# Performance work log

Measured on AMD Instinct MI355X. Metric: run time of the kernel, lower is better.

## Reference

```python
import jax, jax.numpy as jnp
import numpy as np

B, S, E, NH = 2, 2048, 1024, 4
DH = E // NH
EPS = 1e-6  # backend stabilization eps and layernorm eps


def setup_inputs() -> dict:
    key = jax.random.key(0)
    ks = jax.random.split(key, 7)
    q = jax.random.normal(ks[0], (B, S, E), jnp.float32)
    k = jax.random.normal(ks[1], (B, S, E), jnp.float32)
    v = jax.random.normal(ks[2], (B, S, E), jnp.float32)
    # Gate Dense layers: kernel zero-init in the module; use small random so the
    # math is non-trivial. Biases follow the module's inits.
    igate_kernel = 0.02 * jax.random.normal(ks[3], (3 * E, NH), jnp.float32)
    fgate_kernel = 0.02 * jax.random.normal(ks[4], (3 * E, NH), jnp.float32)
    igate_bias = 0.1 * jax.random.normal(ks[5], (NH,), jnp.float32)
    fgate_bias = jnp.linspace(3.0, 6.0, NH, dtype=jnp.float32)  # bias_linspace_init(3,6)
    outnorm_weight = jnp.ones((NH, DH), jnp.float32)
    return {
        "q": q, "k": k, "v": v,
        "igate_kernel": igate_kernel, "igate_bias": igate_bias,
        "fgate_kernel": fgate_kernel, "fgate_bias": fgate_bias,
        "outnorm_weight": outnorm_weight,
    }


def _mlstm_parallel_stabilized(q, k, v, ig, fg):
    # q,k,v: (B,NH,S,DH); ig,fg: (B,NH,S) gate pre-activations
    log_fg = jax.nn.log_sigmoid(fg)                     # (B,NH,S)
    c = jnp.cumsum(log_fg, axis=-1)                     # cumulative forget gates
    # log decay matrix: entry (i,j) = sum_{s=j+1..i} log_fg[s] = c[i]-c[j], causal
    log_fg_mat = c[..., :, None] - c[..., None, :]      # (B,NH,S,S)
    causal = jnp.tril(jnp.ones((S, S), bool))
    log_D = jnp.where(causal, log_fg_mat + ig[..., None, :], -jnp.inf)
    max_log_D = jnp.max(log_D, axis=-1, keepdims=True)  # (B,NH,S,1)
    D = jnp.exp(log_D - max_log_D)                      # stabilized decay matrix
    qk = jnp.einsum("bhsd,bhtd->bhst", q, k) / jnp.sqrt(jnp.float32(DH))
    C = qk * D                                          # (B,NH,S,S)
    normalizer = jnp.maximum(jnp.abs(jnp.sum(C, axis=-1, keepdims=True)),
                             jnp.exp(-max_log_D))
    C_norm = C / (normalizer + EPS)
    return jnp.einsum("bhst,bhtd->bhsd", C_norm, v)     # (B,NH,S,DH)


def reference(q, k, v, igate_kernel, igate_bias, fgate_kernel, fgate_bias, outnorm_weight):
    gate_in = jnp.concatenate([q, k, v], axis=-1)       # (B,S,3E)
    ig = gate_in @ igate_kernel + igate_bias            # (B,S,NH)
    fg = gate_in @ fgate_kernel + fgate_bias            # (B,S,NH)
    qh = q.reshape(B, S, NH, DH).transpose(0, 2, 1, 3)  # (B,NH,S,DH)
    kh = k.reshape(B, S, NH, DH).transpose(0, 2, 1, 3)
    vh = v.reshape(B, S, NH, DH).transpose(0, 2, 1, 3)
    h = _mlstm_parallel_stabilized(qh, kh, vh,
                                   ig.transpose(0, 2, 1), fg.transpose(0, 2, 1))
    h = h.transpose(0, 2, 1, 3)                          # (B,S,NH,DH)
    # MultiHeadLayerNorm: normalize over DH per head, weight only (no bias)
    mean = jnp.mean(h, axis=-1, keepdims=True)
    var = jnp.var(h, axis=-1, keepdims=True)
    h_norm = (h - mean) * jax.lax.rsqrt(var + EPS) * outnorm_weight
    return h_norm.reshape(B, S, E)
```

## Files before the change

### kernel.cpp

```cpp
#include <hip/hip_runtime.h>
#include <hip/hip_bf16.h>
#include <math.h>

#define B_  2
#define S_  2048
#define E_  1024
#define NH_ 4
#define DH_ 256
#define EPSF 1e-6f

typedef __attribute__((ext_vector_type(4)))  short  s16x4;
typedef __attribute__((ext_vector_type(8)))  short  s16x8;
typedef __attribute__((ext_vector_type(8)))  __bf16 bf16x8;
typedef __attribute__((ext_vector_type(4)))  float  f32x4;
typedef __attribute__((ext_vector_type(16))) float  f32x16;

static __device__ __forceinline__ short f2bf(float f) {
    unsigned u = __builtin_bit_cast(unsigned, f);
    u = (u + 0x7FFFu + ((u >> 16) & 1u)) >> 16;
    return (short)u;
}

static __device__ __forceinline__ void gload16(const void* g, void* l) {
    __builtin_amdgcn_global_load_lds(
        (__attribute__((address_space(1))) void*)g,
        (__attribute__((address_space(3))) void*)l, 16, 0, 0);
}

static __device__ __host__ __forceinline__ int chunk_prefix(int N) {
    int k = N >> 3, r = N & 7;
    return 4 * k * (k + 1) + r * (k + 1);
}

__global__ __launch_bounds__(256)
void prep_kernel(const float* __restrict__ q, const float* __restrict__ k,
                 const float* __restrict__ v,
                 const float* __restrict__ igk, const float* __restrict__ igb,
                 const float* __restrict__ fgk, const float* __restrict__ fgb,
                 short* __restrict__ qbf, short* __restrict__ kbf,
                 short* __restrict__ vt,
                 float* __restrict__ ig_ws, float* __restrict__ fg_ws) {
    const int bid = blockIdx.x;
    if (bid < 512) {
        int wid = threadIdx.x >> 6, lane = threadIdx.x & 63;
        int row0 = (bid * 4 + wid) * 2;
        int b = row0 >> 11;
        int s0 = row0 & 2047;
        float accI[2][4] = {};
        float accF[2][4] = {};
        const float* srcs[3] = {q, k, v};
        short* dsts[2] = {qbf, kbf};
#pragma unroll
        for (int p = 0; p < 3; p++) {
            const float* src = srcs[p] + ((long)b * S_ + s0) * E_;
#pragma unroll
            for (int c = 0; c < 4; c++) {
                int e = c * 256 + lane * 4;
                float4 x0 = *(const float4*)(src + e);
                float4 x1 = *(const float4*)(src + E_ + e);
                if (p < 2) {
                    s16x4 o0, o1;
                    o0[0] = f2bf(x0.x); o0[1] = f2bf(x0.y); o0[2] = f2bf(x0.z); o0[3] = f2bf(x0.w);
                    o1[0] = f2bf(x1.x); o1[1] = f2bf(x1.y); o1[2] = f2bf(x1.z); o1[3] = f2bf(x1.w);
                    long db = ((long)(b * NH_ + c) * S_ + s0) * DH_ + lane * 4;
                    *(s16x4*)(dsts[p] + db) = o0;
                    *(s16x4*)(dsts[p] + db + DH_) = o1;
                }
                const float4* wi = (const float4*)(igk + (long)(p * E_ + e) * 4);
                const float4* wf = (const float4*)(fgk + (long)(p * E_ + e) * 4);
                float xs0[4] = {x0.x, x0.y, x0.z, x0.w};
                float xs1[4] = {x1.x, x1.y, x1.z, x1.w};
#pragma unroll
                for (int j = 0; j < 4; j++) {
                    float4 wij = wi[j], wfj = wf[j];
                    accI[0][0] += xs0[j] * wij.x; accI[0][1] += xs0[j] * wij.y;
                    accI[0][2] += xs0[j] * wij.z; accI[0][3] += xs0[j] * wij.w;
                    accF[0][0] += xs0[j] * wfj.x; accF[0][1] += xs0[j] * wfj.y;
                    accF[0][2] += xs0[j] * wfj.z; accF[0][3] += xs0[j] * wfj.w;
                    accI[1][0] += xs1[j] * wij.x; accI[1][1] += xs1[j] * wij.y;
                    accI[1][2] += xs1[j] * wij.z; accI[1][3] += xs1[j] * wij.w;
                    accF[1][0] += xs1[j] * wfj.x; accF[1][1] += xs1[j] * wfj.y;
                    accF[1][2] += xs1[j] * wfj.z; accF[1][3] += xs1[j] * wfj.w;
                }
            }
        }
#pragma unroll
        for (int r = 0; r < 2; r++) {
#pragma unroll
            for (int hh = 0; hh < 4; hh++) {
                float aI = accI[r][hh], aF = accF[r][hh];
                for (int m = 1; m < 64; m <<= 1) { aI += __shfl_xor(aI, m); aF += __shfl_xor(aF, m); }
                if (lane == 0) {
                    ig_ws[((long)(b * NH_ + hh)) * S_ + s0 + r] = aI + igb[hh];
                    fg_ws[((long)(b * NH_ + hh)) * S_ + s0 + r] = aF + fgb[hh];
                }
            }
        }
    } else {
        __shared__ short tile[64][66];
        int b2 = bid - 512;
        int dt = b2 & 3, st = (b2 >> 2) & 31, hh = (b2 >> 7) & 3, b = b2 >> 9;
        int t = threadIdx.x;
#pragma unroll
        for (int rep = 0; rep < 16; rep++) {
            int idx = t + rep * 256;
            int ts = idx >> 6, td = idx & 63;
            float x = v[((long)b * S_ + st * 64 + ts) * E_ + hh * DH_ + dt * 64 + td];
            tile[ts][td] = f2bf(x);
        }
        __syncthreads();
        long obase = ((long)(b * NH_ + hh) * DH_ + dt * 64) * S_ + st * 64;
#pragma unroll
        for (int rep = 0; rep < 8; rep++) {
            int idx = t + rep * 256;
            int dd = idx >> 5, sp = (idx & 31) * 2;
            short2 val;
            val.x = tile[sp][dd];
            val.y = tile[sp + 1][dd];
            *(short2*)(vt + obase + (long)dd * S_ + sp) = val;
        }
    }
}

__global__ __launch_bounds__(256)
void scan_kernel(const float* __restrict__ ig_ws, const float* __restrict__ fg_ws,
                 float* __restrict__ c_ws, float* __restrict__ a_ws,
                 float* __restrict__ M_ws) {
    __shared__ float wsum[4], wmax[4];
    int seq = blockIdx.x;
    int tid = threadIdx.x, w = tid >> 6, lane = tid & 63;
    long base = (long)seq * S_;
    float carryC = 0.f, carryM = -INFINITY;
    for (int ch = 0; ch < S_ / 256; ch++) {
        int s = ch * 256 + tid;
        float fgv = fg_ws[base + s];
        float lf = (fgv > 0.f) ? -log1pf(expf(-fgv)) : (fgv - log1pf(expf(fgv)));
        float x = lf;
        for (int d = 1; d < 64; d <<= 1) { float t = __shfl_up(x, d); if (lane >= d) x += t; }
        if (lane == 63) wsum[w] = x;
        __syncthreads();
        float pre = carryC;
        for (int j = 0; j < w; j++) pre += wsum[j];
        float c = pre + x;
        float a = ig_ws[base + s] - c;
        float m = a;
        for (int d = 1; d < 64; d <<= 1) { float t = __shfl_up(m, d); if (lane >= d) m = fmaxf(m, t); }
        if (lane == 63) wmax[w] = m;
        __syncthreads();
        float prem = carryM;
        for (int j = 0; j < w; j++) prem = fmaxf(prem, wmax[j]);
        float M = fmaxf(prem, m);
        c_ws[base + s] = c;
        a_ws[base + s] = a;
        M_ws[base + s] = M;
        carryC += wsum[0] + wsum[1] + wsum[2] + wsum[3];
        carryM = fmaxf(fmaxf(fmaxf(carryM, wmax[0]), fmaxf(wmax[1], wmax[2])), wmax[3]);
        __syncthreads();
    }
}

__global__ __launch_bounds__(256)
void mlstm_pipe(const short* __restrict__ qbf, const short* __restrict__ kbf,
                const short* __restrict__ vt,
                const float* __restrict__ a_ws, const float* __restrict__ M_ws,
                float* __restrict__ num_ws, float* __restrict__ den_ws) {
    __shared__ __align__(16) char LDSb[139264];

    const int bid = blockIdx.x;
    const int seq = bid & 7;
    const int local = 79 - (bid >> 3);
    int qt = 0;
#pragma unroll
    for (int t = 1; t < 32; t++) if (chunk_prefix(t) <= local) qt = t;
    const int chunk = local - chunk_prefix(qt);
    const int kt0 = chunk * 8;
    const int kt1 = min(kt0 + 8, qt + 1);

    const int tid = threadIdx.x;
    const int w  = tid >> 6;
    const int rg = w & 1;
    const int ct = w >> 1;
    const int l  = tid & 63;
    const int l31 = l & 31;
    const int h5  = l >> 5;

    const long seqbase = (long)seq * S_ * DH_;
    const long gbase = (long)seq * S_;
    const int i0 = qt * 64;

    const char* kseq = (const char*)(kbf + seqbase);
    const char* vseq = (const char*)(vt + seqbase);

    int preK[8], preV[8];
#pragma unroll
    for (int i = 0; i < 8; i++) {
        int r = w * 16 + i * 2 + (l >> 5);
        preK[i] = r * 512 + (((l & 31) * 16) ^ ((r & 7) << 4));
        int d = w * 64 + i * 8 + (l >> 3);
        preV[i] = d * (S_ * 2) + (((l & 7) * 16) ^ ((d & 7) << 4));
    }

    float Mi[16];
#pragma unroll
    for (int reg = 0; reg < 16; reg++) {
        int rowL = 32 * rg + (reg & 3) + 8 * (reg >> 2) + 4 * h5;
        Mi[reg] = M_ws[gbase + i0 + rowL];
    }

    {
        short* Qlds = (short*)LDSb;
#pragma unroll
        for (int rep = 0; rep < 8; rep++) {
            int idx = tid + rep * 256;
            int r = idx >> 5, c = idx & 31;
            s16x8 val = *(const s16x8*)(qbf + seqbase + (long)(i0 + r) * DH_ + c * 8);
            int byte = (r * 512 + c * 16) ^ ((r & 7) << 4);
            *(s16x8*)((char*)Qlds + byte) = val;
        }
    }
    __syncthreads();
    bf16x8 qfrag[16];
    {
        int qrow = 32 * rg + l31;
        int qswz = (qrow & 7) << 4;
#pragma unroll
        for (int dc = 0; dc < 16; dc++)
            qfrag[dc] = *(const bf16x8*)((const char*)LDSb + ((qrow * 512 + dc * 32 + h5 * 16) ^ qswz));
    }
    __syncthreads();

    {
        const char* ks = kseq + (long)kt0 * 64 * 512;
        const char* vs = vseq + (long)kt0 * 128;
        char* kd = LDSb + w * 8192;
        char* vd = LDSb + 65536 + w * 8192;
#pragma unroll
        for (int i = 0; i < 8; i++) gload16(ks + preK[i], kd + i * 1024);
#pragma unroll
        for (int i = 0; i < 8; i++) gload16(vs + preV[i], vd + i * 1024);
    }
    __syncthreads();

    f32x16 oacc[4] = {};
    float denacc[16] = {};

    for (int kt = kt0; kt < kt1; kt++) {
        const int cur = (kt - kt0) & 1;
        const int j0 = kt * 64;

        if (kt + 1 < kt1) {
            const char* ks = kseq + (long)(kt + 1) * 64 * 512;
            const char* vs = vseq + (long)(kt + 1) * 128;
            char* kd = LDSb + (cur ^ 1) * 32768 + w * 8192;
            char* vd = LDSb + 65536 + (cur ^ 1) * 32768 + w * 8192;
#pragma unroll
            for (int i = 0; i < 8; i++) gload16(ks + preK[i], kd + i * 1024);
#pragma unroll
            for (int i = 0; i < 8; i++) gload16(vs + preV[i], vd + i * 1024);
        }

        const char* Klds  = LDSb + cur * 32768;
        const char* Vtlds = LDSb + 65536 + cur * 32768;
        char* Plds = LDSb + 131072;

        float aj = a_ws[gbase + j0 + 32 * ct + l31];

        f32x16 sacc = {};
        {
            int j = 32 * ct + l31;
            int jswz = (j & 7) << 4;
            int jbase = j * 512;
#pragma unroll
            for (int dc = 0; dc < 16; dc++) {
                bf16x8 kf = *(const bf16x8*)(Klds + ((jbase + dc * 32 + h5 * 16) ^ jswz));
                sacc = __builtin_amdgcn_mfma_f32_32x32x16_bf16(qfrag[dc], kf, sacc, 0, 0, 0);
            }
        }

        {
            int jg = j0 + 32 * ct + l31;
#pragma unroll
            for (int reg = 0; reg < 16; reg++) {
                int rowL = 32 * rg + (reg & 3) + 8 * (reg >> 2) + 4 * h5;
                float p = sacc[reg] * 0.0625f * __expf(aj - Mi[reg]);
                if (jg > i0 + rowL) p = 0.f;
                denacc[reg] += p;
                int byte = (rowL * 128 + (32 * ct + l31) * 2) ^ ((rowL & 7) << 4);
                *(short*)(Plds + byte) = f2bf(p);
            }
        }
        __syncthreads();

        bf16x8 pfrag[4];
        {
            int prow = 32 * rg + l31;
            int pswz = (prow & 7) << 4;
#pragma unroll
            for (int k4 = 0; k4 < 4; k4++)
                pfrag[k4] = *(const bf16x8*)(Plds + ((prow * 128 + k4 * 32 + h5 * 16) ^ pswz));
        }
#pragma unroll
        for (int dt = 0; dt < 4; dt++) {
            int d = 128 * ct + 32 * dt + l31;
            int dbase = d * 128, dswz = (d & 7) << 4;
#pragma unroll
            for (int k4 = 0; k4 < 4; k4++) {
                bf16x8 vf = *(const bf16x8*)(Vtlds + ((dbase + k4 * 32 + h5 * 16) ^ dswz));
                oacc[dt] = __builtin_amdgcn_mfma_f32_32x32x16_bf16(pfrag[k4], vf, oacc[dt], 0, 0, 0);
            }
        }
        __syncthreads();
    }

    const long nbase = (long)bid * 64 * 256;
#pragma unroll
    for (int reg = 0; reg < 16; reg++) {
        float dsum = denacc[reg];
        dsum += __shfl_xor(dsum, 1);
        dsum += __shfl_xor(dsum, 2);
        dsum += __shfl_xor(dsum, 4);
        dsum += __shfl_xor(dsum, 8);
        dsum += __shfl_xor(dsum, 16);
        int rowL = 32 * rg + (reg & 3) + 8 * (reg >> 2) + 4 * h5;
        if (l31 == 0) den_ws[(long)bid * 128 + ct * 64 + rowL] = dsum;
    }
#pragma unroll
    for (int dt = 0; dt < 4; dt++) {
#pragma unroll
        for (int reg = 0; reg < 16; reg++) {
            int rowL = 32 * rg + (reg & 3) + 8 * (reg >> 2) + 4 * h5;
            num_ws[nbase + (long)rowL * 256 + 128 * ct + 32 * dt + l31] = oacc[dt][reg];
        }
    }
}

__global__ __launch_bounds__(256)
void reduce_kernel(const float* __restrict__ num_ws, const float* __restrict__ den_ws,
                   const float* __restrict__ c_ws, const float* __restrict__ M_ws,
                   const float* __restrict__ onw, float* __restrict__ out) {
    const int bid = blockIdx.x;
    const int seq = bid & 7;
    const int qh = bid >> 3;
    const int qt = qh >> 1;
    const int half = qh & 1;
    const int h = seq & 3;
    const int b = seq >> 2;
    const int nc = (qt >> 3) + 1;
    const int lbase = chunk_prefix(qt);
    const int w = threadIdx.x >> 6;
    const int l = threadIdx.x & 63;
    const long gbase = (long)seq * S_;

    float4 w4 = *(const float4*)(onw + h * DH_ + l * 4);

    for (int rr = 0; rr < 8; rr++) {
        int row = half * 32 + w * 8 + rr;
        int s = qt * 64 + row;
        float4 acc = {0.f, 0.f, 0.f, 0.f};
        float dsum = 0.f;
        for (int c = 0; c < nc; c++) {
            const long cid = (long)((79 - (lbase + c)) << 3) + seq;
            const float4 p = *(const float4*)(num_ws + cid * 16384 + (long)row * 256 + l * 4);
            acc.x += p.x; acc.y += p.y; acc.z += p.z; acc.w += p.w;
            dsum += den_ws[cid * 128 + row] + den_ws[cid * 128 + 64 + row];
        }
        float lb = __expf(-c_ws[gbase + s] - M_ws[gbase + s]);
        float inv = 1.f / (fmaxf(fabsf(dsum), lb) + EPSF);
        float4 x = {acc.x * inv, acc.y * inv, acc.z * inv, acc.w * inv};
        float sum = x.x + x.y + x.z + x.w;
        sum += __shfl_xor(sum, 1); sum += __shfl_xor(sum, 2); sum += __shfl_xor(sum, 4);
        sum += __shfl_xor(sum, 8); sum += __shfl_xor(sum, 16); sum += __shfl_xor(sum, 32);
        float mean = sum * (1.f / 256.f);
        float vx = x.x - mean, vy = x.y - mean, vz = x.z - mean, vw = x.w - mean;
        float vs = vx * vx + vy * vy + vz * vz + vw * vw;
        vs += __shfl_xor(vs, 1); vs += __shfl_xor(vs, 2); vs += __shfl_xor(vs, 4);
        vs += __shfl_xor(vs, 8); vs += __shfl_xor(vs, 16); vs += __shfl_xor(vs, 32);
        float rstd = rsqrtf(vs * (1.f / 256.f) + EPSF);
        float4 o;
        o.x = vx * rstd * w4.x; o.y = vy * rstd * w4.y;
        o.z = vz * rstd * w4.z; o.w = vw * rstd * w4.w;
        *(float4*)(out + ((long)b * S_ + s) * E_ + h * DH_ + l * 4) = o;
    }
}

__global__ __launch_bounds__(256)
void mlstm_mono(const short* __restrict__ qbf, const short* __restrict__ kbf,
                const short* __restrict__ vt,
                const float* __restrict__ a_ws, const float* __restrict__ M_ws,
                const float* __restrict__ c_ws, const float* __restrict__ onw,
                float* __restrict__ out) {
    __shared__ __align__(16) short Klds[64 * 256];
    __shared__ __align__(16) short Vtlds[256 * 64];
    short* Plds = Klds;

    const int bid = blockIdx.x;
    const int seq = bid & 7;
    const int qt = bid >> 3;
    const int h = seq & 3;
    const int b = seq >> 2;
    const int tid = threadIdx.x;
    const int w = tid >> 6;
    const int l = tid & 63;
    const int l15 = l & 15;
    const int g = l >> 4;

    const long seqbase = (long)seq * S_ * DH_;
    const long gbase = (long)seq * S_;
    const int i0 = qt * 64;

    float Mi_r[4], ci_r[4];
#pragma unroll
    for (int r = 0; r < 4; r++) {
        int il = 16 * w + 4 * g + r;
        Mi_r[r] = M_ws[gbase + i0 + il];
        ci_r[r] = c_ws[gbase + i0 + il];
    }
#pragma unroll
    for (int rep = 0; rep < 8; rep++) {
        int idx = tid + rep * 256;
        int r = idx >> 5, c = idx & 31;
        s16x8 val = *(const s16x8*)(qbf + seqbase + (long)(i0 + r) * DH_ + c * 8);
        int byte = (r * 512 + c * 16) ^ ((r & 7) << 4);
        *(s16x8*)((char*)Klds + byte) = val;
    }
    __syncthreads();
    bf16x8 qfrag[8];
#pragma unroll
    for (int dc = 0; dc < 8; dc++) {
        int r = 16 * w + l15;
        int byte = (r * 512 + (8 * g + 32 * dc) * 2) ^ ((r & 7) << 4);
        qfrag[dc] = *(const bf16x8*)((const char*)Klds + byte);
    }
    __syncthreads();

    const f32x4 fzero = {0.f, 0.f, 0.f, 0.f};
    f32x4 oacc[16];
#pragma unroll
    for (int dt = 0; dt < 16; dt++) oacc[dt] = fzero;
    float den[4] = {0.f, 0.f, 0.f, 0.f};

    const int nkt = qt + 1;
    for (int kt = 0; kt < nkt; kt++) {
        const int j0 = kt * 64;
#pragma unroll
        for (int rep = 0; rep < 8; rep++) {
            int idx = tid + rep * 256;
            int r = idx >> 5, c = idx & 31;
            s16x8 val = *(const s16x8*)(kbf + seqbase + (long)(j0 + r) * DH_ + c * 8);
            int byte = (r * 512 + c * 16) ^ ((r & 7) << 4);
            *(s16x8*)((char*)Klds + byte) = val;
        }
#pragma unroll
        for (int rep = 0; rep < 8; rep++) {
            int idx = tid + rep * 256;
            int d = idx >> 3, c = idx & 7;
            s16x8 val = *(const s16x8*)(vt + seqbase + (long)d * S_ + j0 + c * 8);
            int byte = (d * 128 + c * 16) ^ ((d & 7) << 4);
            *(s16x8*)((char*)Vtlds + byte) = val;
        }
        float aj_ct[4];
#pragma unroll
        for (int ct = 0; ct < 4; ct++) aj_ct[ct] = a_ws[gbase + j0 + 16 * ct + l15];
        __syncthreads();

        f32x4 sacc[4];
#pragma unroll
        for (int ct = 0; ct < 4; ct++) sacc[ct] = fzero;
#pragma unroll
        for (int dc = 0; dc < 8; dc++) {
#pragma unroll
            for (int ct = 0; ct < 4; ct++) {
                int j = 16 * ct + l15;
                int byte = (j * 512 + (8 * g + 32 * dc) * 2) ^ ((j & 7) << 4);
                bf16x8 kf = *(const bf16x8*)((const char*)Klds + byte);
                sacc[ct] = __builtin_amdgcn_mfma_f32_16x16x32_bf16(qfrag[dc], kf, sacc[ct], 0, 0, 0);
            }
        }
        __syncthreads();

        const bool diag = (kt == qt);
#pragma unroll
        for (int ct = 0; ct < 4; ct++) {
            int jl = 16 * ct + l15;
            float aj = aj_ct[ct];
#pragma unroll
            for (int r = 0; r < 4; r++) {
                int il = 16 * w + 4 * g + r;
                float p = sacc[ct][r] * 0.0625f * __expf(aj - Mi_r[r]);
                if (diag && jl > il) p = 0.f;
                den[r] += p;
                int byte = (il * 128 + jl * 2) ^ ((il & 7) << 4);
                *(short*)((char*)Plds + byte) = f2bf(p);
            }
        }
        __syncthreads();

        bf16x8 pfrag[2];
#pragma unroll
        for (int jc = 0; jc < 2; jc++) {
            int i = 16 * w + l15;
            int byte = (i * 128 + (8 * g + 32 * jc) * 2) ^ ((i & 7) << 4);
            pfrag[jc] = *(const bf16x8*)((const char*)Plds + byte);
        }
#pragma unroll
        for (int dt = 0; dt < 16; dt++) {
#pragma unroll
            for (int jc = 0; jc < 2; jc++) {
                int d = 16 * dt + l15;
                int byte = (d * 128 + (8 * g + 32 * jc) * 2) ^ ((d & 7) << 4);
                bf16x8 vf = *(const bf16x8*)((const char*)Vtlds + byte);
                oacc[dt] = __builtin_amdgcn_mfma_f32_16x16x32_bf16(pfrag[jc], vf, oacc[dt], 0, 0, 0);
            }
        }
        __syncthreads();
    }

#pragma unroll
    for (int r = 0; r < 4; r++) {
        float dsum = den[r];
        dsum += __shfl_xor(dsum, 1);
        dsum += __shfl_xor(dsum, 2);
        dsum += __shfl_xor(dsum, 4);
        dsum += __shfl_xor(dsum, 8);
        int il = 16 * w + 4 * g + r;
        float lb = __expf(-ci_r[r] - Mi_r[r]);
        float inv = 1.f / (fmaxf(fabsf(dsum), lb) + EPSF);
        float x[16];
        float sum = 0.f;
#pragma unroll
        for (int dt = 0; dt < 16; dt++) { x[dt] = oacc[dt][r] * inv; sum += x[dt]; }
        sum += __shfl_xor(sum, 1); sum += __shfl_xor(sum, 2);
        sum += __shfl_xor(sum, 4); sum += __shfl_xor(sum, 8);
        float mean = sum * (1.f / 256.f);
        float vs = 0.f;
#pragma unroll
        for (int dt = 0; dt < 16; dt++) { float dx = x[dt] - mean; vs += dx * dx; }
        vs += __shfl_xor(vs, 1); vs += __shfl_xor(vs, 2);
        vs += __shfl_xor(vs, 4); vs += __shfl_xor(vs, 8);
        float rstd = rsqrtf(vs * (1.f / 256.f) + EPSF);
        long orow = ((long)b * S_ + i0 + il) * E_ + h * DH_;
#pragma unroll
        for (int dt = 0; dt < 16; dt++) {
            int d = 16 * dt + l15;
            out[orow + d] = (x[dt] - mean) * rstd * onw[h * DH_ + d];
        }
    }
}

extern "C" void kernel_launch(void* const* d_in, const int* in_sizes, int n_in,
                              void* d_out, int out_size, void* d_ws, size_t ws_size,
                              hipStream_t stream) {
    const float* q   = (const float*)d_in[0];
    const float* k   = (const float*)d_in[1];
    const float* v   = (const float*)d_in[2];
    const float* igk = (const float*)d_in[3];
    const float* igb = (const float*)d_in[4];
    const float* fgk = (const float*)d_in[5];
    const float* fgb = (const float*)d_in[6];
    const float* onw = (const float*)d_in[7];
    float* out = (float*)d_out;

    char* ws = (char*)d_ws;
    float* ig_ws = (float*)(ws);
    float* fg_ws = (float*)(ws + (64  << 10));
    float* c_ws  = (float*)(ws + (128 << 10));
    float* a_ws  = (float*)(ws + (192 << 10));
    float* M_ws  = (float*)(ws + (256 << 10));
    short* qbf   = (short*)(ws + (1L  << 20));
    short* kbf   = (short*)(ws + (9L  << 20));
    short* vtb   = (short*)(ws + (17L << 20));
    float* num_ws = (float*)(ws + (25L << 20));
    float* den_ws = (float*)(ws + (65L << 20));

    prep_kernel<<<1536, 256, 0, stream>>>(q, k, v, igk, igb, fgk, fgb,
                                          qbf, kbf, vtb, ig_ws, fg_ws);
    scan_kernel<<<8, 256, 0, stream>>>(ig_ws, fg_ws, c_ws, a_ws, M_ws);

    if (ws_size >= (66L << 20)) {
        mlstm_pipe  <<<640, 256, 0, stream>>>(qbf, kbf, vtb, a_ws, M_ws, num_ws, den_ws);
        reduce_kernel<<<512, 256, 0, stream>>>(num_ws, den_ws, c_ws, M_ws, onw, out);
    } else {
        mlstm_mono  <<<256, 256, 0, stream>>>(qbf, kbf, vtb, a_ws, M_ws, c_ws, onw, out);
    }
}
```

Baseline: 151.1 us.

## Replace double-buffered K/V staging with single buffer to cut LDS footprint

Drops the double-buffered K/V tiles in shared memory for a single buffer, shrinking LDS from about 136KB to 72KB per block. This could let two blocks share a CU, raising occupancy. The cost is that the prefetch of the next K/V tile no longer overlaps with compute, so each iteration loads and then waits at a barrier before its MFMAs. The hidden loop tail presumably synchronizes before the buffer is overwritten.

```diff
diff --git a/kernel.cpp b/kernel.cpp
--- a/kernel.cpp
+++ b/kernel.cpp
@@ -160,11 +160,11 @@
 }
 
 __global__ __launch_bounds__(256)
-void mlstm_pipe(const short* __restrict__ qbf, const short* __restrict__ kbf,
-                const short* __restrict__ vt,
-                const float* __restrict__ a_ws, const float* __restrict__ M_ws,
-                float* __restrict__ num_ws, float* __restrict__ den_ws) {
-    __shared__ __align__(16) char LDSb[139264];
+void mlstm_sb1(const short* __restrict__ qbf, const short* __restrict__ kbf,
+               const short* __restrict__ vt,
+               const float* __restrict__ a_ws, const float* __restrict__ M_ws,
+               float* __restrict__ num_ws, float* __restrict__ den_ws) {
+    __shared__ __align__(16) char LDSb[73728];
 
     const int bid = blockIdx.x;
     const int seq = bid & 7;
@@ -207,16 +207,13 @@
         Mi[reg] = M_ws[gbase + i0 + rowL];
     }
 
-    {
-        short* Qlds = (short*)LDSb;
-#pragma unroll
-        for (int rep = 0; rep < 8; rep++) {
-            int idx = tid + rep * 256;
-            int r = idx >> 5, c = idx & 31;
-            s16x8 val = *(const s16x8*)(qbf + seqbase + (long)(i0 + r) * DH_ + c * 8);
-            int byte = (r * 512 + c * 16) ^ ((r & 7) << 4);
-            *(s16x8*)((char*)Qlds + byte) = val;
-        }
+#pragma unroll
+    for (int rep = 0; rep < 8; rep++) {
+        int idx = tid + rep * 256;
+        int r = idx >> 5, c = idx & 31;
+        s16x8 val = *(const s16x8*)(qbf + seqbase + (long)(i0 + r) * DH_ + c * 8);
+        int byte = (r * 512 + c * 16) ^ ((r & 7) << 4);
+        *(s16x8*)(LDSb + byte) = val;
     }
     __syncthreads();
     bf16x8 qfrag[16];
@@ -225,45 +222,32 @@
         int qswz = (qrow & 7) << 4;
 #pragma unroll
         for (int dc = 0; dc < 16; dc++)
-            qfrag[dc] = *(const bf16x8*)((const char*)LDSb + ((qrow * 512 + dc * 32 + h5 * 16) ^ qswz));
-    }
-    __syncthreads();
-
-    {
-        const char* ks = kseq + (long)kt0 * 64 * 512;
-        const char* vs = vseq + (long)kt0 * 128;
-        char* kd = LDSb + w * 8192;
-        char* vd = LDSb + 65536 + w * 8192;
-#pragma unroll
-        for (int i = 0; i < 8; i++) gload16(ks + preK[i], kd + i * 1024);
-#pragma unroll
-        for (int i = 0; i < 8; i++) gload16(vs + preV[i], vd + i * 1024);
+            qfrag[dc] = *(const bf16x8*)(LDSb + ((qrow * 512 + dc * 32 + h5 * 16) ^ qswz));
     }
     __syncthreads();
 
     f32x16 oacc[4] = {};
     float denacc[16] = {};
 
+    const char* Klds  = LDSb;
+    const char* Vtlds = LDSb + 32768;
+    char* Plds = LDSb + 65536;
+
     for (int kt = kt0; kt < kt1; kt++) {
-        const int cur = (kt - kt0) & 1;
         const int j0 = kt * 64;
 
-        if (kt + 1 < kt1) {
-            const char* ks = kseq + (long)(kt + 1) * 64 * 512;
-            const char* vs = vseq + (long)(kt + 1) * 128;
-            char* kd = LDSb + (cur ^ 1) * 32768 + w * 8192;
-            char* vd = LDSb + 65536 + (cur ^ 1) * 32768 + w * 8192;
+        {
+            const char* ks = kseq + (long)j0 * 512;
+            const char* vs = vseq + (long)j0 * 2;
+            char* kd = LDSb + w * 8192;
+            char* vd = LDSb + 32768 + w * 8192;
 #pragma unroll
             for (int i = 0; i < 8; i++) gload16(ks + preK[i], kd + i * 1024);
 #pragma unroll
             for (int i = 0; i < 8; i++) gload16(vs + preV[i], vd + i * 1024);
         }
-
-        const char* Klds  = LDSb + cur * 32768;
-        const char* Vtlds = LDSb + 65536 + cur * 32768;
-        char* Plds = LDSb + 131072;
-
         float aj = a_ws[gbase + j0 + 32 * ct + l31];
+        __syncthreads();
 
         f32x16 sacc = {};
         {
@@ -577,7 +561,7 @@
     scan_kernel<<<8, 256, 0, stream>>>(ig_ws, fg_ws, c_ws, a_ws, M_ws);
 
     if (ws_size >= (66L << 20)) {
-        mlstm_pipe  <<<640, 256, 0, stream>>>(qbf, kbf, vtb, a_ws, M_ws, num_ws, den_ws);
+        mlstm_sb1   <<<640, 256, 0, stream>>>(qbf, kbf, vtb, a_ws, M_ws, num_ws, den_ws);
         reduce_kernel<<<512, 256, 0, stream>>>(num_ws, den_ws, c_ws, M_ws, onw, out);
     } else {
         mlstm_mono  <<<256, 256, 0, stream>>>(qbf, kbf, vtb, a_ws, M_ws, c_ws, onw, out);
```

Result: no change. 148.7 us (-1.5%).
